# Performance work log

Measured on AMD Instinct MI355X. Metric: run time of the kernel, lower is better.

## Reference

```python
import jax, jax.numpy as jnp
import numpy as np

T = 1048576      # signal length
K = 3            # number of IMFs
ALPHA = 2000.0   # bandwidth penalty
TAU = 1e-7       # dual ascent step
TOL = 1e-6       # convergence tolerance
N_ITER = 50      # max fixed-point iterations


def _vmd(x, omega_init):
    T_ = x.shape[0]
    t = jnp.arange(1, T_ + 1, dtype=jnp.float32) / T_
    freqs = t - 0.5 - 1.0 / T_                           # [T]
    f_hat = jnp.fft.fftshift(jnp.fft.fft(x))             # [T] complex
    u0 = jnp.zeros((K, T_), dtype=f_hat.dtype)
    lam0 = jnp.zeros((T_,), dtype=f_hat.dtype)

    def step(carry, n):
        u_prev, lam_prev, omega, done = carry
        base = (freqs[None, :] - omega[:, None]) ** 2    # [K,T]
        # mode k's denom also gets (freqs-omega[k-1])^2 and (freqs-omega[k+1])^2
        nbr = jnp.zeros_like(base).at[1:].add(base[:-1]).at[:-1].add(base[1:])
        denom = base + nbr + TAU ** 2
        u_hat = (f_hat[None, :] - lam_prev[None, :] / 2.0) / (1.0 + ALPHA * denom)
        pw = jnp.real(u_hat) ** 2 + jnp.imag(u_hat) ** 2  # |u_hat|^2, [K,T]
        omega_new = jnp.sum(freqs[None, :] * pw, axis=1) / jnp.sum(pw, axis=1)
        lam_new = lam_prev + TAU * (jnp.sum(u_hat, axis=0) - f_hat)
        # convergence check (every 10th iter), mirrors the original break
        u_diff = jnp.sum(jnp.abs(u_hat - u_prev) ** 2) / jnp.sum(jnp.abs(u_prev) ** 2)
        om_diff = jnp.sum(jnp.abs(omega_new - jnp.roll(omega_new, 1))) / K
        conv = (n % 10 == 0) & (u_diff < TOL) & (om_diff < TOL)
        # freeze state once converged (break-iteration's fresh u_hat is kept)
        u_out = jnp.where(done, u_prev, u_hat)
        lam_out = jnp.where(done, lam_prev, lam_new)
        om_out = jnp.where(done, omega, omega_new)
        return (u_out, lam_out, om_out, done | conv), None

    init = (u0, lam0, omega_init.astype(jnp.float32), jnp.array(False))
    (u_hat, _, _, _), _ = jax.lax.scan(jax.checkpoint(step), init, jnp.arange(N_ITER))
    imfs = jnp.real(jnp.fft.ifft(jnp.fft.ifftshift(u_hat, axes=-1), axis=-1))
    return imfs.astype(jnp.float32)                      # [K,T]


def setup_inputs() -> dict:
    key = jax.random.key(0)
    kx, ko = jax.random.split(key)
    x = jax.random.normal(kx, (T,), dtype=jnp.float32)
    omega_init = jax.random.uniform(ko, (K,), dtype=jnp.float32) * 0.5  # init==1
    return {"x": x, "omega_init": omega_init}


def reference(x, omega_init):
    return _vmd(x, omega_init)
```

## Files before the change

kernel.cpp:

```cpp
#include <hip/hip_runtime.h>
#include <math.h>


#define ALPHA_F 2000.0f
#define TAU_F   1e-7f

static __device__ __forceinline__ int lpad2(int i) { return i + (i >> 4); }
static __device__ __forceinline__ int swz(int i)  { return ((i & 7) << 7) | (i >> 3); }
static __device__ __forceinline__ int swzA(int i) { return ((i & 7) << 6) | (i >> 3); }
static __device__ __forceinline__ float frcp(float x) { return __builtin_amdgcn_rcpf(x); }

typedef float v2f __attribute__((ext_vector_type(2)));
static __device__ __forceinline__ v2f sp(float s) { v2f r; r.x = s; r.y = s; return r; }
static __device__ __forceinline__ v2f v2(float a, float b) { v2f r; r.x = a; r.y = b; return r; }
static __device__ __forceinline__ v2f pkfma(v2f a, v2f b, v2f c)
{ return __builtin_elementwise_fma(a, b, c); }
static __device__ __forceinline__ v2f cmul(v2f a, v2f w)
{
  v2f t = a * sp(w.x);
  v2f s = v2(-a.y, a.x);
  return pkfma(s, sp(w.y), t);
}
static __device__ __forceinline__ v2f cmulrr(v2f a, float wr, float wi)
{
  v2f t = a * sp(wr);
  v2f s = v2(-a.y, a.x);
  return pkfma(s, sp(wi), t);
}

#define PADN2 1088

template<int CTRL>
static __device__ __forceinline__ float dpp_addf(float v)
{
  int r = __builtin_amdgcn_update_dpp(0, __float_as_int(v), CTRL, 0xf, 0xf, true);
  return v + __int_as_float(r);
}
static __device__ __forceinline__ float wave64_sum(float v)
{
  v = dpp_addf<0x111>(v);
  v = dpp_addf<0x112>(v);
  v = dpp_addf<0x114>(v);
  v = dpp_addf<0x118>(v);
  v = dpp_addf<0x142>(v);
  v = dpp_addf<0x143>(v);
  return v;
}
static __device__ __forceinline__ float row16_sum(float v)
{
  v = dpp_addf<0x111>(v);
  v = dpp_addf<0x112>(v);
  v = dpp_addf<0x114>(v);
  v = dpp_addf<0x118>(v);
  return v;
}
static __device__ __forceinline__ float rdlane(float v, int l)
{
  return __int_as_float(__builtin_amdgcn_readlane(__float_as_int(v), l));
}

template<int SIGN>
static __device__ void fft1024p(v2f* A, v2f* B)
{
  const int u = threadIdx.x;
  {
    v2f X0 = A[lpad2(u)], X1 = A[lpad2(u + 256)];
    v2f X2 = A[lpad2(u + 512)], X3 = A[lpad2(u + 768)];
    v2f t0 = X0 + X2, t1 = X0 - X2, t2 = X1 + X3, t3 = X1 - X3;
    v2f o0 = t0 + t2, o2 = t0 - t2;
    v2f ns3 = v2(t3.y, -t3.x);
    v2f o1, o3;
    if (SIGN < 0) { o1 = t1 + ns3; o3 = t1 - ns3; }
    else          { o1 = t1 - ns3; o3 = t1 + ns3; }
    const int base = u << 2;
    B[lpad2(base    )] = o0; B[lpad2(base + 1)] = o1;
    B[lpad2(base + 2)] = o2; B[lpad2(base + 3)] = o3;
    __syncthreads();
  }
#pragma unroll
  for (int st = 1; st < 5; ++st) {
    v2f *in  = (st & 1) ? B : A;
    v2f *out = (st & 1) ? A : B;
    const int quarter = 1 << (2 * st);
    const int p = u & (quarter - 1);
    const int g = u >> (2 * st);

    float sw, cw;
    sincospif((float)(2 * p) * (1.0f / (float)(4 << (2 * st))), &sw, &cw);
    const float w1r = cw, w1i = (SIGN < 0) ? -sw : sw;
    const float w2r = w1r * w1r - w1i * w1i, w2i = 2.0f * w1r * w1i;
    const float w3r = w2r * w1r - w2i * w1i, w3i = w2r * w1i + w2i * w1r;

    v2f X0 = in[lpad2(u)], X1 = in[lpad2(u + 256)];
    v2f X2 = in[lpad2(u + 512)], X3 = in[lpad2(u + 768)];

    v2f y1 = cmulrr(X1, w1r, w1i), y2 = cmulrr(X2, w2r, w2i),
        y3 = cmulrr(X3, w3r, w3i);

    v2f t0 = X0 + y2, t1 = X0 - y2, t2 = y1 + y3, t3 = y1 - y3;
    v2f o0 = t0 + t2, o2 = t0 - t2;
    v2f ns3 = v2(t3.y, -t3.x);
    v2f o1, o3;
    if (SIGN < 0) { o1 = t1 + ns3; o3 = t1 - ns3; }
    else          { o1 = t1 - ns3; o3 = t1 + ns3; }

    const int base = (g << (2 * st + 2)) + p;
    out[lpad2(base              )] = o0;
    out[lpad2(base +     quarter)] = o1;
    out[lpad2(base + 2 * quarter)] = o2;
    out[lpad2(base + 3 * quarter)] = o3;
    __syncthreads();
  }
}

__global__ __launch_bounds__(256) void k_fwd_passA(const float* __restrict__ x,
                                                   float2* __restrict__ ws0)
{
  __shared__ __align__(16) v2f A[PADN2], B[PADN2];
  const int p = swzA(blockIdx.x);
  const int tid = threadIdx.x;
  const int c0 = 2 * p;
#pragma unroll
  for (int q = 0; q < 4; ++q) {
    int j = tid + 256 * q;
    A[lpad2(j)] = ((const v2f*)x)[(size_t)j * 512 + p];
  }
  __syncthreads();
  fft1024p<-1>(A, B);

  float sa, ca, sb, cb, ssa, cca, ssb, ccb;
  sincospif((float)(c0 * tid) * (2.0f / 1048576.0f), &sa, &ca);
  sincospif((float)((c0 + 1) * tid) * (2.0f / 1048576.0f), &sb, &cb);
  sincospif((float)c0 * (1.0f / 2048.0f), &ssa, &cca);
  sincospif((float)(c0 + 1) * (1.0f / 2048.0f), &ssb, &ccb);
  v2f E0 = v2(ca, -sa), E1 = v2(cb, -sb);
  const v2f S0 = v2(cca, -ssa), S1 = v2(ccb, -ssb);
#pragma unroll
  for (int q = 0; q < 4; ++q) {
    int k = tid + 256 * q;
    int kk = (1024 - k) & 1023;
    v2f Z = B[lpad2(k)];
    v2f Wv = B[lpad2(kk)];
    float X0r = 0.5f * (Z.x + Wv.x), X0i = 0.5f * (Z.y - Wv.y);
    float X1r = 0.5f * (Z.y + Wv.y), X1i = 0.5f * (Wv.x - Z.x);
    v2f o01 = cmul(v2(X0r, X0i), E0);
    v2f o23 = cmul(v2(X1r, X1i), E1);
    float4 o = make_float4(o01.x, o01.y, o23.x, o23.y);
    ((float4*)ws0)[(size_t)k * 512 + p] = o;
    E0 = cmul(E0, S0); E1 = cmul(E1, S1);
  }
}

__global__ __launch_bounds__(256) void k_fwd_passB(const float2* __restrict__ ws0,
                                                   float2* __restrict__ fhat,
                                                   float* __restrict__ ET)
{
  __shared__ __align__(16) v2f A[PADN2], B[PADN2];
  const int b = swz(blockIdx.x);
  const int tid = threadIdx.x;
#pragma unroll
  for (int q = 0; q < 4; ++q) {
    int j = tid + 256 * q;
    A[lpad2(j)] = ((const v2f*)ws0)[(size_t)b * 1024 + j];
  }
  __syncthreads();
  fft1024p<-1>(A, B);
#pragma unroll
  for (int q = 0; q < 4; ++q) {
    int k2 = tid + 256 * q;
    v2f v = B[lpad2(k2)];
    fhat[(size_t)b * 1024 + k2] = make_float2(v.x, v.y);
    ET[(size_t)k2 * 1024 + b] = v.x * v.x + v.y * v.y;
  }
}

static __device__ __forceinline__ void lag4(float x, float& l0, float& l1,
                                            float& l2, float& l3)
{
  float m0 = x, m1 = x - (1.0f / 3.0f), m2 = x - (2.0f / 3.0f), m3 = x - 1.0f;
  l0 = -4.5f * m1 * m2 * m3;
  l1 = 13.5f * m0 * m2 * m3;
  l2 = -13.5f * m0 * m1 * m3;
  l3 =  4.5f * m0 * m1 * m2;
}

__global__ __launch_bounds__(256) void k_moments(const float* __restrict__ ET,
                                                 double* __restrict__ W)
{
  __shared__ double red[4 * 4];
  const int B = blockIdx.x;
  const int k2 = B ^ 512;
  const int tid = threadIdx.x;
  double a0 = 0, a1 = 0, a2 = 0, a3 = 0;
#pragma unroll
  for (int q = 0; q < 4; ++q) {
    int k1 = tid + 256 * q;
    float e = ET[(size_t)k2 * 1024 + k1];
    float l0, l1, l2, l3;
    lag4((float)k1 * (1.0f / 1024.0f), l0, l1, l2, l3);
    a0 += (double)(e * l0); a1 += (double)(e * l1);
    a2 += (double)(e * l2); a3 += (double)(e * l3);
  }
  const int lane = tid & 63, wv = tid >> 6;
  double pv[4] = { a0, a1, a2, a3 };
#pragma unroll
  for (int j = 0; j < 4; ++j) {
    double v = pv[j];
    for (int off = 32; off; off >>= 1) v += __shfl_down(v, off, 64);
    if (lane == 0) red[wv * 4 + j] = v;
  }
  __syncthreads();
  if (tid < 4)
    W[B * 4 + tid] = red[tid] + red[4 + tid] + red[8 + tid] + red[12 + tid];
}

__global__ __launch_bounds__(1024) void k_solve(
    const double* __restrict__ W4, const float* __restrict__ omega_init,
    float* __restrict__ ckeepN, float* __restrict__ omegaF)
{
  __shared__ float red[2][6 * 16];
  const int t = threadIdx.x;
  const int lane = t & 63, wv = t >> 6;

  float Wsc[4], fsc[4];
#pragma unroll
  for (int e = 0; e < 4; ++e) {
    Wsc[e] = (float)W4[t * 4 + e];
    fsc[e] = (float)((double)t / 1024.0 + (double)e / 3072.0 - 0.5);
  }
  const v2f frP = v2(fsc[0], fsc[1]), frQ = v2(fsc[2], fsc[3]);
  const v2f WrP = v2(Wsc[0], Wsc[1]), WrQ = v2(Wsc[2], Wsc[3]);
  const v2f WfP = WrP * frP,          WfQ = WrQ * frQ;
  v2f cnrP = sp(0.0f), cnrQ = sp(0.0f);

  float om0 = omega_init[0], om1 = omega_init[1], om2 = omega_init[2];

#pragma unroll 1
  for (int it = 0; it < 49; ++it) {
    float* rb = red[it & 1];
    v2f p0 = sp(0.f), p1 = sp(0.f), p2 = sp(0.f),
        p3 = sp(0.f), p4 = sp(0.f), p5 = sp(0.f);

    auto node_pair = [&](const v2f fv, const v2f Wrv, const v2f Wfv, v2f& cnv) {
      v2f a0 = fv - sp(om0), a1 = fv - sp(om1), a2 = fv - sp(om2);
      v2f d0 = a0 * a0, d1 = a1 * a1, d2 = a2 * a2;
      v2f s01 = d0 + d1, s12 = d1 + d2;
      v2f dA = pkfma(sp(ALPHA_F), s01, sp(1.0f));
      v2f dC = pkfma(sp(ALPHA_F), s12, sp(1.0f));
      v2f dB = pkfma(sp(ALPHA_F), d2, dA);
      v2f AB = dA * dB, BC = dB * dC, AC = dA * dC;
      v2f ABC = AB * dC;
      v2f r = v2(frcp(ABC.x), frcp(ABC.y));
      v2f w0 = BC * r, w1 = AC * r, w2 = AB * r;
      v2f hf = pkfma(sp(-0.5f), cnv, sp(1.0f));
      v2f g = hf * hf;
      v2f gw0 = g * (w0 * w0), gw1 = g * (w1 * w1), gw2 = g * (w2 * w2);
      p0 = pkfma(Wfv, gw0, p0); p1 = pkfma(Wfv, gw1, p1); p2 = pkfma(Wfv, gw2, p2);
      p3 = pkfma(Wrv, gw0, p3); p4 = pkfma(Wrv, gw1, p4); p5 = pkfma(Wrv, gw2, p5);
      v2f S = (w0 + w1) + w2;
      cnv = pkfma(sp(TAU_F), pkfma(S, hf, sp(-1.0f)), cnv);
    };
    node_pair(frP, WrP, WfP, cnrP);
    node_pair(frQ, WrQ, WfQ, cnrQ);

    float q0 = p0.x + p0.y, q1 = p1.x + p1.y, q2 = p2.x + p2.y;
    float q3 = p3.x + p3.y, q4 = p4.x + p4.y, q5 = p5.x + p5.y;

    q0 = wave64_sum(q0); q1 = wave64_sum(q1); q2 = wave64_sum(q2);
    q3 = wave64_sum(q3); q4 = wave64_sum(q4); q5 = wave64_sum(q5);
    if (lane == 63) {
      rb[0 * 16 + wv] = q0; rb[1 * 16 + wv] = q1; rb[2 * 16 + wv] = q2;
      rb[3 * 16 + wv] = q3; rb[4 * 16 + wv] = q4; rb[5 * 16 + wv] = q5;
    }
    __syncthreads();
    float v1 = rb[lane];
    float v2_ = rb[64 + (lane & 31)];
    v1 = row16_sum(v1);
    v2_ = row16_sum(v2_);
    float n0 = rdlane(v1, 15), n1 = rdlane(v1, 31), n2 = rdlane(v1, 47);
    float e0 = rdlane(v1, 63), e1 = rdlane(v2_, 15), e2 = rdlane(v2_, 31);
    om0 = n0 * frcp(e0);
    om1 = n1 * frcp(e1);
    om2 = n2 * frcp(e2);
  }

  ((float4*)ckeepN)[t] = make_float4(cnrP.x, cnrP.y, cnrQ.x, cnrQ.y);
  if (t == 0) { omegaF[0] = om0; omegaF[1] = om1; omegaF[2] = om2; }
}

__global__ __launch_bounds__(256) void k_inv_A2(
    const float2* __restrict__ fhat, const float* __restrict__ ckeepN,
    const float* __restrict__ omegaF, float2* __restrict__ ws0)
{
  __shared__ __align__(16) v2f A[PADN2], B[PADN2];
  __shared__ float cn4[4096];
  __shared__ float som[3];
  const int tid = threadIdx.x;
  const int b = swz(blockIdx.x);
  for (int i = tid; i < 4096; i += 256) cn4[i] = ckeepN[i];
  if (tid == 0) { som[0] = omegaF[0]; som[1] = omegaF[1]; som[2] = omegaF[2]; }
  __syncthreads();
  const float om0 = som[0], om1 = som[1], om2 = som[2];
  const float xb = (float)b * (1.0f / 1024.0f);
  float l0, l1, l2, l3, m0, m1, m2, m3;
  lag4(xb, l0, l1, l2, l3);
  lag4(1.0f - xb, m0, m1, m2, m3);

  v2f v2reg[4];
#pragma unroll
  for (int q = 0; q < 4; ++q) {
    int j = tid + 256 * q;
    float2 f = fhat[(size_t)b * 1024 + j];
    int bin = j ^ 512;
    int binp = 1023 - bin;
    float4 cv = ((const float4*)cn4)[bin];
    float4 cw = ((const float4*)cn4)[binp];
    float c  = l0 * cv.x + l1 * cv.y + l2 * cv.z + l3 * cv.w;
    float cp = m0 * cw.x + m1 * cw.y + m2 * cw.z + m3 * cw.w;
    float hf = 1.0f - 0.5f * c;
    float hp = 1.0f - 0.5f * cp;
    int tt = (bin << 10) | b;
    float freq = (float)tt * (1.0f / 1048576.0f) - 0.5f;
    v2f fpm = v2(freq, -freq);
    v2f A0 = fpm - sp(om0), A1 = fpm - sp(om1), A2v = fpm - sp(om2);
    v2f D0 = A0 * A0, D1 = A1 * A1, D2 = A2v * A2v;
    v2f DA = pkfma(sp(ALPHA_F), D0 + D1, sp(1.0f));
    v2f DB = pkfma(sp(ALPHA_F), D2, DA);
    float r0 = hf * frcp(DA.x), r0n = hp * frcp(DA.y);
    float r1 = hf * frcp(DB.x), r1n = hp * frcp(DB.y);
    float Rr = 0.5f * (r0 + r0n), Ri = 0.5f * (r1 + r1n);
    A[lpad2(j)] = cmul(v2(f.x, f.y), v2(Rr, Ri));
    v2f DC = pkfma(sp(ALPHA_F), D1 + D2, sp(1.0f));
    float r2 = hf * frcp(DC.x), r2n = hp * frcp(DC.y);
    float Rr2 = 0.5f * (r2 + r2n);
    v2reg[q] = v2(f.x, f.y) * sp(Rr2);
  }
  __syncthreads();
  fft1024p<1>(A, B);

  float sa, ca, ss, cs;
  sincospif((float)(b * tid) * (2.0f / 1048576.0f), &sa, &ca);
  sincospif((float)b * (1.0f / 2048.0f), &ss, &cs);
  const v2f Einit = v2(ca, sa);
  const v2f S = v2(cs, ss);

  v2f E = Einit;
#pragma unroll
  for (int q = 0; q < 4; ++q) {
    int m1i = tid + 256 * q;
    v2f v = B[lpad2(m1i)];
    v2f o = cmul(v, E);
    ws0[(size_t)m1i * 1024 + b] = make_float2(o.x, o.y);
    E = cmul(E, S);
    A[lpad2(m1i)] = v2reg[q];
  }
  __syncthreads();
  fft1024p<1>(A, B);

  E = Einit;
#pragma unroll
  for (int q = 0; q < 4; ++q) {
    int m1i = tid + 256 * q;
    v2f v = B[lpad2(m1i)];
    v2f o = cmul(v, E);
    ws0[1048576 + (size_t)m1i * 1024 + b] = make_float2(o.x, o.y);
    E = cmul(E, S);
  }
}

__global__ __launch_bounds__(256) void k_inv_B2(const float2* __restrict__ ws0,
                                                float* __restrict__ out)
{
  __shared__ __align__(16) v2f A[PADN2], B[PADN2];
  const int pk = blockIdx.x >> 10;
  const int b = swz(blockIdx.x & 1023);
  const int tid = threadIdx.x;
#pragma unroll
  for (int q = 0; q < 4; ++q) {
    int j = tid + 256 * q;
    A[lpad2(j)] = ((const v2f*)ws0)[(size_t)pk * 1048576 + (size_t)b * 1024 + j];
  }
  __syncthreads();
  fft1024p<1>(A, B);
  const float sc = 1.0f / 1048576.0f;
#pragma unroll
  for (int q = 0; q < 4; ++q) {
    int m2 = tid + 256 * q;
    v2f v = B[lpad2(m2)];
    if (pk == 0) {
      out[(size_t)m2 * 1024 + b]           = v.x * sc;
      out[1048576 + (size_t)m2 * 1024 + b] = v.y * sc;
    } else {
      out[2097152 + (size_t)m2 * 1024 + b] = v.x * sc;
    }
  }
}

extern "C" void kernel_launch(void* const* d_in, const int* in_sizes, int n_in,
                              void* d_out, int out_size, void* d_ws, size_t ws_size,
                              hipStream_t stream)
{
  (void)in_sizes; (void)n_in; (void)out_size; (void)ws_size;
  const float* x       = (const float*)d_in[0];
  const float* om_init = (const float*)d_in[1];
  float* out = (float*)d_out;

  char* w = (char*)d_ws;
  const size_t MB = 1024ull * 1024ull;
  float2* fhat     = (float2*)(w);
  float*  ET       = (float*)(w + 8 * MB);
  double* W4       = (double*)(w + 12 * MB);
  float*  ckeepN   = (float*)(w + 12 * MB + 32 * 1024);
  float*  omegaF   = (float*)(w + 12 * MB + 48 * 1024);
  float2* scratch  = (float2*)(w + 16 * MB);

  k_fwd_passA<<<512, 256, 0, stream>>>(x, scratch);
  k_fwd_passB<<<1024, 256, 0, stream>>>(scratch, fhat, ET);
  k_moments<<<1024, 256, 0, stream>>>(ET, W4);
  k_solve<<<1, 1024, 0, stream>>>(W4, om_init, ckeepN, omegaF);
  k_inv_A2<<<1024, 256, 0, stream>>>(fhat, ckeepN, omegaF, scratch);
  k_inv_B2<<<2048, 256, 0, stream>>>(scratch, out);
}
```

Before: 183.2 us.

## Feed FFT first stage from registers and pack third IMF real-output transforms in pairs

The 1024-point FFT helper now takes its first-stage inputs in registers, which removes one shared-memory store/load round trip and one barrier per FFT in every pass. The final inverse pass for the third mode uses the real-output property: it combines two columns into one complex FFT via Hermitian symmetrisation, so that pass needs half the blocks (1536 instead of 2048). The cn4 table load in k_inv_A2 is also vectorised to float4. In exchange there is more register pressure and extra shared-memory loads for the symmetrisation step.

```diff
diff --git a/kernel.cpp b/kernel.cpp
--- a/kernel.cpp
+++ b/kernel.cpp
@@ -60,12 +60,11 @@
 }
 
 template<int SIGN>
-static __device__ void fft1024p(v2f* A, v2f* B)
+static __device__ void fft1024p_reg(v2f X0, v2f X1, v2f X2, v2f X3,
+                                    v2f* A, v2f* B)
 {
   const int u = threadIdx.x;
   {
-    v2f X0 = A[lpad2(u)], X1 = A[lpad2(u + 256)];
-    v2f X2 = A[lpad2(u + 512)], X3 = A[lpad2(u + 768)];
     v2f t0 = X0 + X2, t1 = X0 - X2, t2 = X1 + X3, t3 = X1 - X3;
     v2f o0 = t0 + t2, o2 = t0 - t2;
     v2f ns3 = v2(t3.y, -t3.x);
@@ -91,13 +90,13 @@
     const float w2r = w1r * w1r - w1i * w1i, w2i = 2.0f * w1r * w1i;
     const float w3r = w2r * w1r - w2i * w1i, w3i = w2r * w1i + w2i * w1r;
 
-    v2f X0 = in[lpad2(u)], X1 = in[lpad2(u + 256)];
-    v2f X2 = in[lpad2(u + 512)], X3 = in[lpad2(u + 768)];
-
-    v2f y1 = cmulrr(X1, w1r, w1i), y2 = cmulrr(X2, w2r, w2i),
-        y3 = cmulrr(X3, w3r, w3i);
-
-    v2f t0 = X0 + y2, t1 = X0 - y2, t2 = y1 + y3, t3 = y1 - y3;
+    v2f Y0 = in[lpad2(u)], Y1 = in[lpad2(u + 256)];
+    v2f Y2 = in[lpad2(u + 512)], Y3 = in[lpad2(u + 768)];
+
+    v2f y1 = cmulrr(Y1, w1r, w1i), y2 = cmulrr(Y2, w2r, w2i),
+        y3 = cmulrr(Y3, w3r, w3i);
+
+    v2f t0 = Y0 + y2, t1 = Y0 - y2, t2 = y1 + y3, t3 = y1 - y3;
     v2f o0 = t0 + t2, o2 = t0 - t2;
     v2f ns3 = v2(t3.y, -t3.x);
     v2f o1, o3;
@@ -120,13 +119,11 @@
   const int p = swzA(blockIdx.x);
   const int tid = threadIdx.x;
   const int c0 = 2 * p;
-#pragma unroll
-  for (int q = 0; q < 4; ++q) {
-    int j = tid + 256 * q;
-    A[lpad2(j)] = ((const v2f*)x)[(size_t)j * 512 + p];
-  }
-  __syncthreads();
-  fft1024p<-1>(A, B);
+  v2f X[4];
+#pragma unroll
+  for (int q = 0; q < 4; ++q)
+    X[q] = ((const v2f*)x)[(size_t)(tid + 256 * q) * 512 + p];
+  fft1024p_reg<-1>(X[0], X[1], X[2], X[3], A, B);
 
   float sa, ca, sb, cb, ssa, cca, ssb, ccb;
   sincospif((float)(c0 * tid) * (2.0f / 1048576.0f), &sa, &ca);
@@ -158,13 +155,11 @@
   __shared__ __align__(16) v2f A[PADN2], B[PADN2];
   const int b = swz(blockIdx.x);
   const int tid = threadIdx.x;
-#pragma unroll
-  for (int q = 0; q < 4; ++q) {
-    int j = tid + 256 * q;
-    A[lpad2(j)] = ((const v2f*)ws0)[(size_t)b * 1024 + j];
-  }
-  __syncthreads();
-  fft1024p<-1>(A, B);
+  v2f X[4];
+#pragma unroll
+  for (int q = 0; q < 4; ++q)
+    X[q] = ((const v2f*)ws0)[(size_t)b * 1024 + tid + 256 * q];
+  fft1024p_reg<-1>(X[0], X[1], X[2], X[3], A, B);
 #pragma unroll
   for (int q = 0; q < 4; ++q) {
     int k2 = tid + 256 * q;
@@ -297,7 +292,8 @@
   __shared__ float som[3];
   const int tid = threadIdx.x;
   const int b = swz(blockIdx.x);
-  for (int i = tid; i < 4096; i += 256) cn4[i] = ckeepN[i];
+  for (int i = tid; i < 1024; i += 256)
+    ((float4*)cn4)[i] = ((const float4*)ckeepN)[i];
   if (tid == 0) { som[0] = omegaF[0]; som[1] = omegaF[1]; som[2] = omegaF[2]; }
   __syncthreads();
   const float om0 = som[0], om1 = som[1], om2 = som[2];
@@ -306,6 +302,7 @@
   lag4(xb, l0, l1, l2, l3);
   lag4(1.0f - xb, m0, m1, m2, m3);
 
+  v2f X[4];
   v2f v2reg[4];
 #pragma unroll
   for (int q = 0; q < 4; ++q) {
@@ -329,14 +326,13 @@
     float r0 = hf * frcp(DA.x), r0n = hp * frcp(DA.y);
     float r1 = hf * frcp(DB.x), r1n = hp * frcp(DB.y);
     float Rr = 0.5f * (r0 + r0n), Ri = 0.5f * (r1 + r1n);
-    A[lpad2(j)] = cmul(v2(f.x, f.y), v2(Rr, Ri));
+    X[q] = cmul(v2(f.x, f.y), v2(Rr, Ri));
     v2f DC = pkfma(sp(ALPHA_F), D1 + D2, sp(1.0f));
     float r2 = hf * frcp(DC.x), r2n = hp * frcp(DC.y);
     float Rr2 = 0.5f * (r2 + r2n);
     v2reg[q] = v2(f.x, f.y) * sp(Rr2);
   }
-  __syncthreads();
-  fft1024p<1>(A, B);
+  fft1024p_reg<1>(X[0], X[1], X[2], X[3], A, B);
 
   float sa, ca, ss, cs;
   sincospif((float)(b * tid) * (2.0f / 1048576.0f), &sa, &ca);
@@ -352,10 +348,9 @@
     v2f o = cmul(v, E);
     ws0[(size_t)m1i * 1024 + b] = make_float2(o.x, o.y);
     E = cmul(E, S);
-    A[lpad2(m1i)] = v2reg[q];
   }
   __syncthreads();
-  fft1024p<1>(A, B);
+  fft1024p_reg<1>(v2reg[0], v2reg[1], v2reg[2], v2reg[3], A, B);
 
   E = Einit;
 #pragma unroll
@@ -372,26 +367,52 @@
                                                 float* __restrict__ out)
 {
   __shared__ __align__(16) v2f A[PADN2], B[PADN2];
-  const int pk = blockIdx.x >> 10;
-  const int b = swz(blockIdx.x & 1023);
   const int tid = threadIdx.x;
-#pragma unroll
-  for (int q = 0; q < 4; ++q) {
-    int j = tid + 256 * q;
-    A[lpad2(j)] = ((const v2f*)ws0)[(size_t)pk * 1048576 + (size_t)b * 1024 + j];
-  }
-  __syncthreads();
-  fft1024p<1>(A, B);
   const float sc = 1.0f / 1048576.0f;
-#pragma unroll
-  for (int q = 0; q < 4; ++q) {
-    int m2 = tid + 256 * q;
-    v2f v = B[lpad2(m2)];
-    if (pk == 0) {
+
+  if (blockIdx.x < 1024) {
+    const int b = swz(blockIdx.x);
+    v2f X[4];
+#pragma unroll
+    for (int q = 0; q < 4; ++q)
+      X[q] = ((const v2f*)ws0)[(size_t)b * 1024 + tid + 256 * q];
+    fft1024p_reg<1>(X[0], X[1], X[2], X[3], A, B);
+#pragma unroll
+    for (int q = 0; q < 4; ++q) {
+      int m2 = tid + 256 * q;
+      v2f v = B[lpad2(m2)];
       out[(size_t)m2 * 1024 + b]           = v.x * sc;
       out[1048576 + (size_t)m2 * 1024 + b] = v.y * sc;
-    } else {
-      out[2097152 + (size_t)m2 * 1024 + b] = v.x * sc;
+    }
+  } else {
+    const int s = swzA(blockIdx.x - 1024);
+    const int b0 = 2 * s, b1 = 2 * s + 1;
+#pragma unroll
+    for (int q = 0; q < 4; ++q) {
+      int j = tid + 256 * q;
+      A[lpad2(j)] = ((const v2f*)ws0)[1048576 + (size_t)b0 * 1024 + j];
+      B[lpad2(j)] = ((const v2f*)ws0)[1048576 + (size_t)b1 * 1024 + j];
+    }
+    __syncthreads();
+    v2f Z[4];
+#pragma unroll
+    for (int q = 0; q < 4; ++q) {
+      int j = tid + 256 * q;
+      int mj = (1024 - j) & 1023;
+      v2f W0j = A[lpad2(j)], W0m = A[lpad2(mj)];
+      v2f W1j = B[lpad2(j)], W1m = B[lpad2(mj)];
+      float H0r = 0.5f * (W0j.x + W0m.x), H0i = 0.5f * (W0j.y - W0m.y);
+      float H1r = 0.5f * (W1j.x + W1m.x), H1i = 0.5f * (W1j.y - W1m.y);
+      Z[q] = v2(H0r - H1i, H0i + H1r);
+    }
+    __syncthreads();
+    fft1024p_reg<1>(Z[0], Z[1], Z[2], Z[3], A, B);
+#pragma unroll
+    for (int q = 0; q < 4; ++q) {
+      int m2 = tid + 256 * q;
+      v2f v = B[lpad2(m2)];
+      out[2097152 + (size_t)m2 * 1024 + b0] = v.x * sc;
+      out[2097152 + (size_t)m2 * 1024 + b1] = v.y * sc;
     }
   }
 }
@@ -419,5 +440,5 @@
   k_moments<<<1024, 256, 0, stream>>>(ET, W4);
   k_solve<<<1, 1024, 0, stream>>>(W4, om_init, ckeepN, omegaF);
   k_inv_A2<<<1024, 256, 0, stream>>>(fhat, ckeepN, omegaF, scratch);
-  k_inv_B2<<<2048, 256, 0, stream>>>(scratch, out);
-}
+  k_inv_B2<<<1536, 256, 0, stream>>>(scratch, out);
+}
```

After: 178.8 us. 1.02x faster.
